# Performance work log

Measured on AMD Instinct MI355X. Metric: run time of the kernel, lower is better.

## Reference

```python
import jax, jax.numpy as jnp
import numpy as np

B, N, IN_DIM, HID, OUT, HEADS = 2, 1024, 64, 64, 64, 4
PHD1, PHD2 = HID // HEADS, OUT // HEADS
SLOPE = 0.2  # PyG GATv2Conv default negative_slope
EPS = 1e-12  # F.normalize eps


def _gatv2_dense(x, Wl, Wr, att, bias, heads, phd, mask):
    """Dense GATv2 layer over a full adjacency mask.
    x: [B,N,Din]; Wl/Wr: [Din, heads*phd]; att: [heads,phd]; bias: [heads*phd];
    mask: [N,N] bool, mask[i,j]=True means edge j->i exists.
    """
    Bb, Nn, _ = x.shape
    xl = (x @ Wl).reshape(Bb, Nn, heads, phd)  # source features
    xr = (x @ Wr).reshape(Bb, Nn, heads, phd)  # target features
    # s[b,i,j,h,p] = leaky_relu(xr[b,i] + xl[b,j])  (GATv2)
    s = jax.nn.leaky_relu(xr[:, :, None] + xl[:, None, :], SLOPE)
    e = jnp.einsum('bijhp,hp->bijh', s, att)  # [B,Ni,Nj,H]
    e = jnp.where(mask[None, :, :, None], e, -jnp.inf)
    alpha = jax.nn.softmax(e, axis=2)  # softmax over source nodes j
    out = jnp.einsum('bijh,bjhp->bihp', alpha, xl).reshape(Bb, Nn, heads * phd)
    return out + bias


def setup_inputs() -> dict:
    key = jax.random.key(0)
    ks = jax.random.split(key, 10)
    sc = 0.1
    return {
        'x': jax.random.normal(ks[0], (B, N, IN_DIM), jnp.float32),
        'embedding': jax.random.normal(ks[1], (N, HID), jnp.float32),
        'Wl1': jax.random.normal(ks[2], (IN_DIM, HEADS * PHD1), jnp.float32) * sc,
        'Wr1': jax.random.normal(ks[3], (IN_DIM, HEADS * PHD1), jnp.float32) * sc,
        'att1': jax.random.normal(ks[4], (HEADS, PHD1), jnp.float32) * sc,
        'b1': jnp.zeros((HEADS * PHD1,), jnp.float32),
        'Wl2': jax.random.normal(ks[5], (HID, HEADS * PHD2), jnp.float32) * sc,
        'Wr2': jax.random.normal(ks[6], (HID, HEADS * PHD2), jnp.float32) * sc,
        'att2': jax.random.normal(ks[7], (HEADS, PHD2), jnp.float32) * sc,
        'b2': jnp.zeros((HEADS * PHD2,), jnp.float32),
    }


def reference(x, embedding, Wl1, Wr1, att1, b1, Wl2, Wr2, att2, b2):
    # AdaptiveAdjacency: cosine-similarity adjacency; only its nonzero pattern is used.
    norm = jnp.maximum(jnp.linalg.norm(embedding, axis=1, keepdims=True), EPS)
    ne = embedding / norm
    adj = ne @ ne.T  # [N,N]
    # edge set = adj.nonzero(); GATv2Conv(add_self_loops=True) guarantees diagonal
    mask = (adj != 0) | jnp.eye(N, dtype=bool)
    h = jax.nn.relu(_gatv2_dense(x, Wl1, Wr1, att1, b1, HEADS, PHD1, mask))
    # dropout(0.3) in eval mode -> identity
    return _gatv2_dense(h, Wl2, Wr2, att2, b2, HEADS, PHD2, mask)
```

## Files before the change

kernel.cpp:

```cpp
#include <hip/hip_runtime.h>
#include <math.h>

#define NN 1024
#define BB 2
#define D 64
#define NHEAD 4
#define PH 16
#define LOG2E 1.4426950408889634f

template <int CTRL>
__device__ __forceinline__ float dpp_mov(float x) {
    int xi = __builtin_bit_cast(int, x);
    int r = __builtin_amdgcn_update_dpp(0, xi, CTRL, 0xF, 0xF, true);
    return __builtin_bit_cast(float, r);
}

__device__ __forceinline__ float dpp_rowsum16(float t) {
    t += dpp_mov<0x111>(t);
    t += dpp_mov<0x112>(t);
    t += dpp_mov<0x114>(t);
    t += dpp_mov<0x118>(t);
    return t;
}

__device__ __forceinline__ float quad_sum4(float t) {
    t += dpp_mov<0xB1>(t);
    t += dpp_mov<0x4E>(t);
    return t;
}

#define MST 65
__global__ __launch_bounds__(256) void k_mask(const float* __restrict__ emb,
                                              unsigned char* __restrict__ mask) {
    __shared__ float As[64 * MST];
    __shared__ float Bs[64 * MST];
    int tid = threadIdx.x;
    int ib = (blockIdx.x & 15) << 6;
    int jb = (blockIdx.x >> 4) << 6;

    #pragma unroll
    for (int r = 0; r < 4; ++r) {
        int q = tid + (r << 8);
        int row = q >> 4, c4 = (q & 15) << 2;
        float4 a = *(const float4*)&emb[(ib + row) * D + c4];
        float4 b = *(const float4*)&emb[(jb + row) * D + c4];
        As[row * MST + c4 + 0] = a.x; As[row * MST + c4 + 1] = a.y;
        As[row * MST + c4 + 2] = a.z; As[row * MST + c4 + 3] = a.w;
        Bs[row * MST + c4 + 0] = b.x; Bs[row * MST + c4 + 1] = b.y;
        Bs[row * MST + c4 + 2] = b.z; Bs[row * MST + c4 + 3] = b.w;
    }
    __syncthreads();

    int i0 = (tid >> 4) << 2;
    int j0 = (tid & 15) << 2;
    float acc[4][4] = {};
    #pragma unroll 8
    for (int k = 0; k < 64; ++k) {
        float a0 = As[(i0 + 0) * MST + k];
        float a1 = As[(i0 + 1) * MST + k];
        float a2 = As[(i0 + 2) * MST + k];
        float a3 = As[(i0 + 3) * MST + k];
        float b0 = Bs[(j0 + 0) * MST + k];
        float b1 = Bs[(j0 + 1) * MST + k];
        float b2 = Bs[(j0 + 2) * MST + k];
        float b3 = Bs[(j0 + 3) * MST + k];
        acc[0][0] = fmaf(a0, b0, acc[0][0]); acc[0][1] = fmaf(a0, b1, acc[0][1]);
        acc[0][2] = fmaf(a0, b2, acc[0][2]); acc[0][3] = fmaf(a0, b3, acc[0][3]);
        acc[1][0] = fmaf(a1, b0, acc[1][0]); acc[1][1] = fmaf(a1, b1, acc[1][1]);
        acc[1][2] = fmaf(a1, b2, acc[1][2]); acc[1][3] = fmaf(a1, b3, acc[1][3]);
        acc[2][0] = fmaf(a2, b0, acc[2][0]); acc[2][1] = fmaf(a2, b1, acc[2][1]);
        acc[2][2] = fmaf(a2, b2, acc[2][2]); acc[2][3] = fmaf(a2, b3, acc[2][3]);
        acc[3][0] = fmaf(a3, b0, acc[3][0]); acc[3][1] = fmaf(a3, b1, acc[3][1]);
        acc[3][2] = fmaf(a3, b2, acc[3][2]); acc[3][3] = fmaf(a3, b3, acc[3][3]);
    }
    #pragma unroll
    for (int r = 0; r < 4; ++r) {
        int gi = ib + i0 + r;
        uchar4 m;
        m.x = (acc[r][0] != 0.f || gi == jb + j0 + 0) ? 1 : 0;
        m.y = (acc[r][1] != 0.f || gi == jb + j0 + 1) ? 1 : 0;
        m.z = (acc[r][2] != 0.f || gi == jb + j0 + 2) ? 1 : 0;
        m.w = (acc[r][3] != 0.f || gi == jb + j0 + 3) ? 1 : 0;
        *(uchar4*)&mask[gi * NN + jb + j0] = m;
    }
}

__global__ __launch_bounds__(256) void k_gemm2(const float* __restrict__ A,
                                               const float* __restrict__ Wl,
                                               const float* __restrict__ Wr,
                                               const float* __restrict__ att,
                                               float* __restrict__ xl,
                                               float* __restrict__ xr,
                                               float* __restrict__ alE) {
    __shared__ float wl[64 * 64];
    __shared__ float wr[64 * 64];
    int tid = threadIdx.x;
    for (int t = tid; t < 4096; t += 256) { wl[t] = Wl[t]; wr[t] = Wr[t]; }
    __syncthreads();
    int r = blockIdx.x * 4 + (tid >> 6);
    int c = tid & 63;
    float av = att[c];
    const float* arow = A + r * 64;
    float accl = 0.f, accr = 0.f;
    #pragma unroll
    for (int p = 0; p < 64; ++p) {
        float a = arow[p];
        accl = fmaf(a, wl[p * 64 + c], accl);
        accr = fmaf(a, wr[p * 64 + c], accr);
    }
    xl[r * 64 + c] = accl;
    xr[r * 64 + c] = accr;
    float t = dpp_rowsum16(accl * av);
    if ((c & 15) == 15) alE[(r << 2) | (c >> 4)] = 0.6f * LOG2E * t;
}

template <bool RELU>
__global__ __launch_bounds__(256, 4) void k_attn(
    const float* __restrict__ xl, const float* __restrict__ xr,
    const float* __restrict__ att, const float* __restrict__ alE,
    const float* __restrict__ bias, const unsigned char* __restrict__ mask,
    float* __restrict__ out)
{
    __shared__ float Opart[2][4][4][64];
    __shared__ float Lpart[2][4][4][NHEAD];

    int tid = threadIdx.x;
    int wave = tid >> 6, lane = tid & 63;
    int h = lane & 3, jl = lane >> 2;
    int b = blockIdx.x >> 9;
    int i0 = (blockIdx.x & 511) << 1;
    int j0 = (wave << 8) + (jl << 4);

    const float* xlb = xl + (b << 16);

    float at[16], xr0f[16], xr1f[16];
    {
        const float* ap = att + (h << 2);
        const float* r0 = xr + (((b << 10) + i0) << 6) + (h << 2);
        const float* r1 = r0 + 64;
        #pragma unroll
        for (int q = 0; q < 4; ++q) {
            *(float4*)&at[q << 2]   = *(const float4*)(ap + (q << 4));
            *(float4*)&xr0f[q << 2] = *(const float4*)(r0 + (q << 4));
            *(float4*)&xr1f[q << 2] = *(const float4*)(r1 + (q << 4));
        }
        #pragma unroll
        for (int p = 0; p < 16; ++p) at[p] *= 0.4f * LOG2E;
    }
    float ar0q[4], ar1q[4];
    #pragma unroll
    for (int q = 0; q < 4; ++q) {
        float p0 = 0.f, p1 = 0.f;
        #pragma unroll
        for (int r = 0; r < 4; ++r) {
            p0 = fmaf(at[(q << 2) + r], xr0f[(q << 2) + r], p0);
            p1 = fmaf(at[(q << 2) + r], xr1f[(q << 2) + r], p1);
        }
        ar0q[q] = 1.5f * quad_sum4(p0);
        ar1q[q] = 1.5f * quad_sum4(p1);
    }

    unsigned mb0 = 0, mb1 = 0;
    {
        const unsigned* m0p = (const unsigned*)(mask + i0 * NN + j0);
        const unsigned* m1p = (const unsigned*)(mask + (i0 + 1) * NN + j0);
        #pragma unroll
        for (int q = 0; q < 4; ++q) {
            unsigned w0 = m0p[q], w1 = m1p[q];
            mb0 |= ((((w0 >> 0) & 1) | ((w0 >> 7) & 2) | ((w0 >> 14) & 4) | ((w0 >> 21) & 8)) << (q << 2));
            mb1 |= ((((w1 >> 0) & 1) | ((w1 >> 7) & 2) | ((w1 >> 14) & 4) | ((w1 >> 21) & 8)) << (q << 2));
        }
    }

    float O0[16], O1[16], l0q[4] = {}, l1q[4] = {};
    #pragma unroll
    for (int p = 0; p < 16; ++p) { O0[p] = 0.f; O1[p] = 0.f; }

    const float* xrow = xlb + (j0 << 6) + (h << 2);
    const float* alp  = alE + (b << 12) + (j0 << 2);

    #pragma unroll 2
    for (int s = 0; s < 16; ++s) {
        const float* rp = xrow + (s << 6);
        float xv[16];
        *(float4*)&xv[0]  = *(const float4*)(rp);
        *(float4*)&xv[4]  = *(const float4*)(rp + 16);
        *(float4*)&xv[8]  = *(const float4*)(rp + 32);
        *(float4*)&xv[12] = *(const float4*)(rp + 48);
        float alr[4];
        *(float4*)alr = *(const float4*)(alp + (s << 2));
        bool m0 = (mb0 >> s) & 1, m1 = (mb1 >> s) & 1;

        #pragma unroll
        for (int q = 0; q < 4; ++q) {
            float p0 = 0.f, p1 = 0.f;
            #pragma unroll
            for (int r = 0; r < 4; ++r) {
                float xvv = xv[(q << 2) + r];
                float a = at[(q << 2) + r];
                p0 = fmaf(a, __builtin_fabsf(xr0f[(q << 2) + r] + xvv), p0);
                p1 = fmaf(a, __builtin_fabsf(xr1f[(q << 2) + r] + xvv), p1);
            }
            float e0 = quad_sum4(p0) + (ar0q[q] + alr[q]);
            float e1 = quad_sum4(p1) + (ar1q[q] + alr[q]);
            float pe0 = m0 ? __builtin_amdgcn_exp2f(e0) : 0.f;
            float pe1 = m1 ? __builtin_amdgcn_exp2f(e1) : 0.f;
            l0q[q] += pe0;
            l1q[q] += pe1;
            #pragma unroll
            for (int r = 0; r < 4; ++r) {
                float xvv = xv[(q << 2) + r];
                O0[(q << 2) + r] = fmaf(pe0, xvv, O0[(q << 2) + r]);
                O1[(q << 2) + r] = fmaf(pe1, xvv, O1[(q << 2) + r]);
            }
        }
    }

    #pragma unroll
    for (int p = 0; p < 16; ++p) {
        O0[p] += dpp_mov<0x114>(O0[p]);  O0[p] += dpp_mov<0x118>(O0[p]);
        O1[p] += dpp_mov<0x114>(O1[p]);  O1[p] += dpp_mov<0x118>(O1[p]);
    }
    #pragma unroll
    for (int q = 0; q < 4; ++q) {
        l0q[q] += dpp_mov<0x114>(l0q[q]);  l0q[q] += dpp_mov<0x118>(l0q[q]);
        l1q[q] += dpp_mov<0x114>(l1q[q]);  l1q[q] += dpp_mov<0x118>(l1q[q]);
    }

    if ((lane & 15) >= 12) {
        int k = lane >> 4;
        #pragma unroll
        for (int q = 0; q < 4; ++q) {
            *(float4*)&Opart[0][wave][k][(q << 4) + (h << 2)] = *(const float4*)&O0[q << 2];
            *(float4*)&Opart[1][wave][k][(q << 4) + (h << 2)] = *(const float4*)&O1[q << 2];
        }
        if (h == 0) {
            #pragma unroll
            for (int q = 0; q < 4; ++q) {
                Lpart[0][wave][k][q] = l0q[q];
                Lpart[1][wave][k][q] = l1q[q];
            }
        }
    }
    __syncthreads();

    if (tid < 128) {
        int ii = tid >> 6, c = tid & 63;
        float o = 0.f, l = 0.f;
        #pragma unroll
        for (int w = 0; w < 4; ++w)
            #pragma unroll
            for (int k = 0; k < 4; ++k) {
                o += Opart[ii][w][k][c];
                l += Lpart[ii][w][k][c >> 4];
            }
        float res = o / l + bias[c];
        if (RELU) res = fmaxf(res, 0.f);
        out[((b << 10) + i0 + ii) * D + c] = res;
    }
}

extern "C" void kernel_launch(void* const* d_in, const int* in_sizes, int n_in,
                              void* d_out, int out_size, void* d_ws, size_t ws_size,
                              hipStream_t stream) {
    const float* x    = (const float*)d_in[0];
    const float* emb  = (const float*)d_in[1];
    const float* Wl1  = (const float*)d_in[2];
    const float* Wr1  = (const float*)d_in[3];
    const float* att1 = (const float*)d_in[4];
    const float* b1   = (const float*)d_in[5];
    const float* Wl2  = (const float*)d_in[6];
    const float* Wr2  = (const float*)d_in[7];
    const float* att2 = (const float*)d_in[8];
    const float* b2   = (const float*)d_in[9];
    float* out = (float*)d_out;

    unsigned char* mask = (unsigned char*)d_ws;
    float* xl = (float*)(mask + NN * NN);
    float* xr = xl + BB * NN * D;
    float* hbuf = xr + BB * NN * D;
    float* alE = hbuf + BB * NN * D;

    k_mask<<<256, 256, 0, stream>>>(emb, mask);

    k_gemm2<<<BB * NN / 4, 256, 0, stream>>>(x, Wl1, Wr1, att1, xl, xr, alE);
    k_attn<true><<<BB * NN / 2, 256, 0, stream>>>(xl, xr, att1, alE, b1, mask, hbuf);

    k_gemm2<<<BB * NN / 4, 256, 0, stream>>>(hbuf, Wl2, Wr2, att2, xl, xr, alE);
    k_attn<false><<<BB * NN / 2, 256, 0, stream>>>(xl, xr, att2, alE, b2, mask, out);
}
```

Baseline: 144.9 us.

## Process four target rows per attention block and double-buffer source loads

Each attention block now handles four target nodes instead of two, so every loaded source row (xl, alE) is reused across four rows and half as many blocks are launched. The inner loop is restructured with explicit A/B register double-buffering so the next tile's loads are issued before the current tile is computed. Launch bounds drop from 4 to 2 blocks per SM to make room for the larger per-thread accumulator state, which lowers occupancy and halves the grid, leaving fewer blocks to spread across the device.

```diff
diff --git a/kernel.cpp b/kernel.cpp
--- a/kernel.cpp
+++ b/kernel.cpp
@@ -115,136 +115,155 @@
 }
 
 template <bool RELU>
-__global__ __launch_bounds__(256, 4) void k_attn(
+__global__ __launch_bounds__(256, 2) void k_attn(
     const float* __restrict__ xl, const float* __restrict__ xr,
     const float* __restrict__ att, const float* __restrict__ alE,
     const float* __restrict__ bias, const unsigned char* __restrict__ mask,
     float* __restrict__ out)
 {
-    __shared__ float Opart[2][4][4][64];
-    __shared__ float Lpart[2][4][4][NHEAD];
+    __shared__ float Opart[4][4][4][64];
+    __shared__ float Lpart[4][4][4][NHEAD];
 
     int tid = threadIdx.x;
     int wave = tid >> 6, lane = tid & 63;
     int h = lane & 3, jl = lane >> 2;
-    int b = blockIdx.x >> 9;
-    int i0 = (blockIdx.x & 511) << 1;
+    int b = blockIdx.x >> 8;
+    int i0 = (blockIdx.x & 255) << 2;
     int j0 = (wave << 8) + (jl << 4);
 
     const float* xlb = xl + (b << 16);
 
-    float at[16], xr0f[16], xr1f[16];
+    float at[16];
+    float xrf[4][16];
     {
         const float* ap = att + (h << 2);
-        const float* r0 = xr + (((b << 10) + i0) << 6) + (h << 2);
-        const float* r1 = r0 + 64;
+        #pragma unroll
+        for (int q = 0; q < 4; ++q)
+            *(float4*)&at[q << 2] = *(const float4*)(ap + (q << 4));
+        #pragma unroll
+        for (int p = 0; p < 16; ++p) at[p] *= 0.4f * LOG2E;
+        #pragma unroll
+        for (int rw = 0; rw < 4; ++rw) {
+            const float* rp = xr + (((b << 10) + i0 + rw) << 6) + (h << 2);
+            #pragma unroll
+            for (int q = 0; q < 4; ++q)
+                *(float4*)&xrf[rw][q << 2] = *(const float4*)(rp + (q << 4));
+        }
+    }
+    float arq[4][4];
+    #pragma unroll
+    for (int rw = 0; rw < 4; ++rw) {
         #pragma unroll
         for (int q = 0; q < 4; ++q) {
-            *(float4*)&at[q << 2]   = *(const float4*)(ap + (q << 4));
-            *(float4*)&xr0f[q << 2] = *(const float4*)(r0 + (q << 4));
-            *(float4*)&xr1f[q << 2] = *(const float4*)(r1 + (q << 4));
-        }
-        #pragma unroll
-        for (int p = 0; p < 16; ++p) at[p] *= 0.4f * LOG2E;
-    }
-    float ar0q[4], ar1q[4];
-    #pragma unroll
-    for (int q = 0; q < 4; ++q) {
-        float p0 = 0.f, p1 = 0.f;
-        #pragma unroll
-        for (int r = 0; r < 4; ++r) {
-            p0 = fmaf(at[(q << 2) + r], xr0f[(q << 2) + r], p0);
-            p1 = fmaf(at[(q << 2) + r], xr1f[(q << 2) + r], p1);
-        }
-        ar0q[q] = 1.5f * quad_sum4(p0);
-        ar1q[q] = 1.5f * quad_sum4(p1);
-    }
-
-    unsigned mb0 = 0, mb1 = 0;
-    {
-        const unsigned* m0p = (const unsigned*)(mask + i0 * NN + j0);
-        const unsigned* m1p = (const unsigned*)(mask + (i0 + 1) * NN + j0);
+            float p0 = 0.f;
+            #pragma unroll
+            for (int r = 0; r < 4; ++r)
+                p0 = fmaf(at[(q << 2) + r], xrf[rw][(q << 2) + r], p0);
+            arq[rw][q] = 1.5f * quad_sum4(p0);
+        }
+    }
+
+    unsigned mb[4];
+    #pragma unroll
+    for (int rw = 0; rw < 4; ++rw) {
+        const unsigned* mp = (const unsigned*)(mask + (i0 + rw) * NN + j0);
+        unsigned acc = 0;
         #pragma unroll
         for (int q = 0; q < 4; ++q) {
-            unsigned w0 = m0p[q], w1 = m1p[q];
-            mb0 |= ((((w0 >> 0) & 1) | ((w0 >> 7) & 2) | ((w0 >> 14) & 4) | ((w0 >> 21) & 8)) << (q << 2));
-            mb1 |= ((((w1 >> 0) & 1) | ((w1 >> 7) & 2) | ((w1 >> 14) & 4) | ((w1 >> 21) & 8)) << (q << 2));
-        }
-    }
-
-    float O0[16], O1[16], l0q[4] = {}, l1q[4] = {};
-    #pragma unroll
-    for (int p = 0; p < 16; ++p) { O0[p] = 0.f; O1[p] = 0.f; }
+            unsigned w = mp[q];
+            acc |= ((((w >> 0) & 1) | ((w >> 7) & 2) | ((w >> 14) & 4) | ((w >> 21) & 8)) << (q << 2));
+        }
+        mb[rw] = acc;
+    }
+
+    float O[4][16];
+    float lq[4][4];
+    #pragma unroll
+    for (int rw = 0; rw < 4; ++rw) {
+        #pragma unroll
+        for (int p = 0; p < 16; ++p) O[rw][p] = 0.f;
+        #pragma unroll
+        for (int q = 0; q < 4; ++q) lq[rw][q] = 0.f;
+    }
 
     const float* xrow = xlb + (j0 << 6) + (h << 2);
     const float* alp  = alE + (b << 12) + (j0 << 2);
 
-    #pragma unroll 2
-    for (int s = 0; s < 16; ++s) {
+    auto loadt = [&](float (&xv)[16], float (&alr)[4], int s) {
         const float* rp = xrow + (s << 6);
-        float xv[16];
         *(float4*)&xv[0]  = *(const float4*)(rp);
         *(float4*)&xv[4]  = *(const float4*)(rp + 16);
         *(float4*)&xv[8]  = *(const float4*)(rp + 32);
         *(float4*)&xv[12] = *(const float4*)(rp + 48);
-        float alr[4];
         *(float4*)alr = *(const float4*)(alp + (s << 2));
-        bool m0 = (mb0 >> s) & 1, m1 = (mb1 >> s) & 1;
-
+    };
+
+    auto compute = [&](const float (&xv)[16], const float (&alr)[4], int s) {
         #pragma unroll
         for (int q = 0; q < 4; ++q) {
-            float p0 = 0.f, p1 = 0.f;
-            #pragma unroll
-            for (int r = 0; r < 4; ++r) {
-                float xvv = xv[(q << 2) + r];
-                float a = at[(q << 2) + r];
-                p0 = fmaf(a, __builtin_fabsf(xr0f[(q << 2) + r] + xvv), p0);
-                p1 = fmaf(a, __builtin_fabsf(xr1f[(q << 2) + r] + xvv), p1);
+            float pp[4];
+            #pragma unroll
+            for (int rw = 0; rw < 4; ++rw) {
+                float t = 0.f;
+                #pragma unroll
+                for (int r = 0; r < 4; ++r)
+                    t = fmaf(at[(q << 2) + r],
+                             __builtin_fabsf(xrf[rw][(q << 2) + r] + xv[(q << 2) + r]), t);
+                pp[rw] = t;
             }
-            float e0 = quad_sum4(p0) + (ar0q[q] + alr[q]);
-            float e1 = quad_sum4(p1) + (ar1q[q] + alr[q]);
-            float pe0 = m0 ? __builtin_amdgcn_exp2f(e0) : 0.f;
-            float pe1 = m1 ? __builtin_amdgcn_exp2f(e1) : 0.f;
-            l0q[q] += pe0;
-            l1q[q] += pe1;
-            #pragma unroll
-            for (int r = 0; r < 4; ++r) {
-                float xvv = xv[(q << 2) + r];
-                O0[(q << 2) + r] = fmaf(pe0, xvv, O0[(q << 2) + r]);
-                O1[(q << 2) + r] = fmaf(pe1, xvv, O1[(q << 2) + r]);
+            #pragma unroll
+            for (int rw = 0; rw < 4; ++rw) {
+                float e = quad_sum4(pp[rw]) + (arq[rw][q] + alr[q]);
+                float pe = ((mb[rw] >> s) & 1) ? __builtin_amdgcn_exp2f(e) : 0.f;
+                lq[rw][q] += pe;
+                #pragma unroll
+                for (int r = 0; r < 4; ++r)
+                    O[rw][(q << 2) + r] = fmaf(pe, xv[(q << 2) + r], O[rw][(q << 2) + r]);
             }
         }
-    }
-
-    #pragma unroll
-    for (int p = 0; p < 16; ++p) {
-        O0[p] += dpp_mov<0x114>(O0[p]);  O0[p] += dpp_mov<0x118>(O0[p]);
-        O1[p] += dpp_mov<0x114>(O1[p]);  O1[p] += dpp_mov<0x118>(O1[p]);
-    }
-    #pragma unroll
-    for (int q = 0; q < 4; ++q) {
-        l0q[q] += dpp_mov<0x114>(l0q[q]);  l0q[q] += dpp_mov<0x118>(l0q[q]);
-        l1q[q] += dpp_mov<0x114>(l1q[q]);  l1q[q] += dpp_mov<0x118>(l1q[q]);
+    };
+
+    float xvA[16], alrA[4], xvB[16], alrB[4];
+    loadt(xvA, alrA, 0);
+    #pragma unroll
+    for (int s = 0; s < 16; s += 2) {
+        loadt(xvB, alrB, s + 1);
+        compute(xvA, alrA, s);
+        if (s + 2 < 16) loadt(xvA, alrA, s + 2);
+        compute(xvB, alrB, s + 1);
+    }
+
+    #pragma unroll
+    for (int rw = 0; rw < 4; ++rw) {
+        #pragma unroll
+        for (int p = 0; p < 16; ++p) {
+            O[rw][p] += dpp_mov<0x114>(O[rw][p]);
+            O[rw][p] += dpp_mov<0x118>(O[rw][p]);
+        }
+        #pragma unroll
+        for (int q = 0; q < 4; ++q) {
+            lq[rw][q] += dpp_mov<0x114>(lq[rw][q]);
+            lq[rw][q] += dpp_mov<0x118>(lq[rw][q]);
+        }
     }
 
     if ((lane & 15) >= 12) {
         int k = lane >> 4;
         #pragma unroll
-        for (int q = 0; q < 4; ++q) {
-            *(float4*)&Opart[0][wave][k][(q << 4) + (h << 2)] = *(const float4*)&O0[q << 2];
-            *(float4*)&Opart[1][wave][k][(q << 4) + (h << 2)] = *(const float4*)&O1[q << 2];
-        }
-        if (h == 0) {
-            #pragma unroll
-            for (int q = 0; q < 4; ++q) {
-                Lpart[0][wave][k][q] = l0q[q];
-                Lpart[1][wave][k][q] = l1q[q];
+        for (int rw = 0; rw < 4; ++rw) {
+            #pragma unroll
+            for (int q = 0; q < 4; ++q)
+                *(float4*)&Opart[rw][wave][k][(q << 4) + (h << 2)] = *(const float4*)&O[rw][q << 2];
+            if (h == 0) {
+                #pragma unroll
+                for (int q = 0; q < 4; ++q)
+                    Lpart[rw][wave][k][q] = lq[rw][q];
             }
         }
     }
     __syncthreads();
 
-    if (tid < 128) {
+    {
         int ii = tid >> 6, c = tid & 63;
         float o = 0.f, l = 0.f;
         #pragma unroll
@@ -284,8 +303,8 @@
     k_mask<<<256, 256, 0, stream>>>(emb, mask);
 
     k_gemm2<<<BB * NN / 4, 256, 0, stream>>>(x, Wl1, Wr1, att1, xl, xr, alE);
-    k_attn<true><<<BB * NN / 2, 256, 0, stream>>>(xl, xr, att1, alE, b1, mask, hbuf);
+    k_attn<true><<<BB * NN / 4, 256, 0, stream>>>(xl, xr, att1, alE, b1, mask, hbuf);
 
     k_gemm2<<<BB * NN / 4, 256, 0, stream>>>(hbuf, Wl2, Wr2, att2, xl, xr, alE);
-    k_attn<false><<<BB * NN / 2, 256, 0, stream>>>(xl, xr, att2, alE, b2, mask, out);
-}
+    k_attn<false><<<BB * NN / 4, 256, 0, stream>>>(xl, xr, att2, alE, b2, mask, out);
+}
```

Result: slower. 358.9 us (+147.7%).
